# Kernel optimization log

Measured on AMD Instinct MI355X. Metric: run time of the kernel, lower is better.

## Reference

```python
import jax, jax.numpy as jnp
import numpy as np

T = 0.4       # gumbel temperature (self.T)
BASE = 3.0    # sigmoid offset (self.base)
LN_EPS = 1e-5


def setup_inputs() -> dict:
    key = jax.random.key(0)
    ks = jax.random.split(key, 4)
    B, S, D = 2, 2048, 4096
    E, EMB, M = 64, 128, 11008
    return {
        "x": jax.random.normal(ks[0], (B, S, D), dtype=jnp.float32),
        "rnn_state": jax.random.normal(ks[1], (E, EMB), dtype=jnp.float32),
        "Wr": jax.random.normal(ks[2], (E, D), dtype=jnp.float32) * 0.02,
        "Wd": jax.random.normal(ks[3], (M, EMB), dtype=jnp.float32) * 0.02,
        "ln_w": jnp.ones((EMB,), dtype=jnp.float32),
        "ln_b": jnp.zeros((EMB,), dtype=jnp.float32),
    }


def _layernorm(h, w, b):
    mu = jnp.mean(h, axis=-1, keepdims=True)
    var = jnp.var(h, axis=-1, keepdims=True)
    return (h - mu) * jax.lax.rsqrt(var + LN_EPS) * w + b


def reference(x, rnn_state, Wr, Wd, ln_w, ln_b):
    key = jax.random.key(42)
    k1, k2 = jax.random.split(key)
    # router logits: [B, S, E]
    logits = jnp.einsum("bsd,ed->bse", x, Wr)
    # ST gumbel-softmax (hard one-hot routing)
    eps = 1e-20
    u = jax.random.uniform(k1, logits.shape, dtype=logits.dtype)
    g = -jnp.log(-jnp.log(u + eps) + eps)
    y_soft = jax.nn.softmax((logits + g) / T, axis=-1)
    y_hard = jax.nn.one_hot(jnp.argmax(y_soft, axis=-1), logits.shape[-1], dtype=y_soft.dtype)
    router = jax.lax.stop_gradient(y_hard - y_soft) + y_soft
    # gather routed embedding: [B, S, EMB]
    routed = jnp.einsum("bse,ec->bsc", router, rnn_state)
    # LN + GELU (exact erf) + decode: [B, S, M]
    h = jax.nn.gelu(_layernorm(routed, ln_w, ln_b), approximate=False)
    pre = jnp.einsum("bsc,mc->bsm", h, Wd)
    # ST gumbel-sigmoid with offset, hard round
    e = jax.random.exponential(k2, pre.shape, dtype=pre.dtype)
    gum = -jnp.log(e)
    b_soft = jax.nn.sigmoid((pre + gum + BASE) / T)
    b_hard = jnp.round(b_soft)
    binary = jax.lax.stop_gradient(b_hard - b_soft) + b_soft
    return (binary, router)
```

## Files before the change

### kernel.cpp

```cpp
#include <hip/hip_runtime.h>
#include <hip/hip_bf16.h>
#include <stdint.h>

typedef float floatx4 __attribute__((ext_vector_type(4)));

__host__ __device__ inline void tf2x32(uint32_t k0, uint32_t k1,
                                       uint32_t x0, uint32_t x1,
                                       uint32_t& o0, uint32_t& o1) {
  const uint32_t k2 = k0 ^ k1 ^ 0x1BD11BDAu;
  x0 += k0; x1 += k1;
#define TFR(r) { x0 += x1; x1 = ((x1 << (r)) | (x1 >> (32 - (r)))); x1 ^= x0; }
  TFR(13) TFR(15) TFR(26) TFR(6)
  x0 += k1; x1 += k2 + 1u;
  TFR(17) TFR(29) TFR(16) TFR(24)
  x0 += k2; x1 += k0 + 2u;
  TFR(13) TFR(15) TFR(26) TFR(6)
  x0 += k0; x1 += k1 + 3u;
  TFR(17) TFR(29) TFR(16) TFR(24)
  x0 += k1; x1 += k2 + 4u;
  TFR(13) TFR(15) TFR(26) TFR(6)
  x0 += k2; x1 += k0 + 5u;
#undef TFR
  o0 = x0; o1 = x1;
}

__device__ inline uint32_t jax_bits32(uint32_t kA, uint32_t kB, uint32_t i) {
  uint32_t o0, o1;
  tf2x32(kA, kB, 0u, i, o0, o1);
  return o0 ^ o1;
}

__device__ inline float jax_uniform(uint32_t bits) {
  return __uint_as_float((bits >> 9) | 0x3f800000u) - 1.0f;
}

#define D_DIM   4096
#define E_DIM   64
#define EMB     128
#define M_DIM   11008
#define NROWS   4096
#define BIN_N   45088768
#define BK      32

__global__ __launch_bounds__(256) void krnA(const float* __restrict__ x,
                                            const float* __restrict__ Wr,
                                            float* __restrict__ part) {
  __shared__ float xs[64][BK + 1];
  __shared__ float wrs[64][BK + 1];
  const int rt = blockIdx.x, ks = blockIdx.y, t = threadIdx.x;
  const int row0 = rt * 64, k0 = ks * 1024;
  const int i = t >> 4, j = t & 15;
  float acc[4][4] = {};
  for (int kt = 0; kt < 1024; kt += BK) {
#pragma unroll
    for (int it = 0; it < 2; ++it) {
      int idx = t + it * 256;
      int r = idx >> 3, kq = idx & 7;
      float4 v = *(const float4*)&x[(size_t)(row0 + r) * D_DIM + k0 + kt + kq * 4];
      xs[r][kq * 4 + 0] = v.x; xs[r][kq * 4 + 1] = v.y;
      xs[r][kq * 4 + 2] = v.z; xs[r][kq * 4 + 3] = v.w;
      float4 w = *(const float4*)&Wr[(size_t)r * D_DIM + k0 + kt + kq * 4];
      wrs[r][kq * 4 + 0] = w.x; wrs[r][kq * 4 + 1] = w.y;
      wrs[r][kq * 4 + 2] = w.z; wrs[r][kq * 4 + 3] = w.w;
    }
    __syncthreads();
#pragma unroll
    for (int k = 0; k < BK; ++k) {
      float xv[4], wv[4];
#pragma unroll
      for (int c = 0; c < 4; ++c) xv[c] = xs[i * 4 + c][k];
#pragma unroll
      for (int d = 0; d < 4; ++d) wv[d] = wrs[j * 4 + d][k];
#pragma unroll
      for (int c = 0; c < 4; ++c)
#pragma unroll
        for (int d = 0; d < 4; ++d) acc[c][d] += xv[c] * wv[d];
    }
    __syncthreads();
  }
  float* pp = part + ((size_t)ks * NROWS + row0) * E_DIM;
#pragma unroll
  for (int c = 0; c < 4; ++c)
#pragma unroll
    for (int d = 0; d < 4; ++d)
      pp[(i * 4 + c) * E_DIM + j * 4 + d] = acc[c][d];
}

__global__ __launch_bounds__(256) void krnB(const float* __restrict__ part,
                                            float* __restrict__ router_out,
                                            int* __restrict__ eidx,
                                            uint32_t K1A, uint32_t K1B) {
  const int t = threadIdx.x;
  const int wv = t >> 6, lane = t & 63;
  const int row = blockIdx.x * 4 + wv;
  float lg = 0.0f;
#pragma unroll
  for (int s = 0; s < 4; ++s)
    lg += part[((size_t)s * NROWS + row) * E_DIM + lane];

  uint32_t jf = (uint32_t)row * 64u + (uint32_t)lane;
  uint32_t bits = jax_bits32(K1A, K1B, jf);
  float u = jax_uniform(bits);
  float inner = -logf(u + 1e-20f);
  float g = -logf(inner + 1e-20f);
  float w = (lg + g) * 2.5f;

  float m = w;
#pragma unroll
  for (int off = 32; off >= 1; off >>= 1) m = fmaxf(m, __shfl_xor(m, off));
  unsigned long long msk = __ballot(w == m);
  int arg = __ffsll(msk) - 1;
  router_out[(size_t)row * E_DIM + lane] = (lane == arg) ? 1.0f : 0.0f;
  if (lane == 0) eidx[row] = arg;
}

__global__ __launch_bounds__(64) void krnC1(const float* __restrict__ rnn,
                                            const float* __restrict__ lnw,
                                            const float* __restrict__ lnb,
                                            float* __restrict__ H) {
  const int r = blockIdx.x, lane = threadIdx.x;
  float v0 = rnn[r * EMB + lane], v1 = rnn[r * EMB + 64 + lane];
  float s = v0 + v1;
#pragma unroll
  for (int off = 32; off >= 1; off >>= 1) s += __shfl_xor(s, off);
  float mu = s * (1.0f / 128.0f);
  float d0 = v0 - mu, d1 = v1 - mu;
  float q = d0 * d0 + d1 * d1;
#pragma unroll
  for (int off = 32; off >= 1; off >>= 1) q += __shfl_xor(q, off);
  float var = q * (1.0f / 128.0f);
  float rs = rsqrtf(var + 1e-5f);
  float h0 = d0 * rs * lnw[lane] + lnb[lane];
  float h1 = d1 * rs * lnw[lane + 64] + lnb[lane + 64];
  float g0 = 0.5f * h0 * (1.0f + erff(h0 * 0.70710678118654752f));
  float g1 = 0.5f * h1 * (1.0f + erff(h1 * 0.70710678118654752f));
  H[r * EMB + lane] = g0;
  H[r * EMB + 64 + lane] = g1;
}

__global__ __launch_bounds__(256) void krnC2(const float* __restrict__ H,
                                             const float* __restrict__ Wd,
                                             float* __restrict__ P) {
  __shared__ float4 hs[64][32];
  const int t = threadIdx.x;
#pragma unroll
  for (int it = 0; it < 8; ++it) {
    int idx = t + it * 256;
    hs[idx >> 5][idx & 31] = ((const float4*)H)[idx];
  }
  __syncthreads();
  const int wv = t >> 6, lane = t & 63;
  const int m = blockIdx.x * 64 + lane;
  const float4* wd4 = (const float4*)(Wd + (size_t)m * EMB);
  float acc[16] = {};
  for (int c4 = 0; c4 < 32; ++c4) {
    float4 w = wd4[c4];
#pragma unroll
    for (int e = 0; e < 16; ++e) {
      float4 h = hs[wv * 16 + e][c4];
      acc[e] += w.x * h.x + w.y * h.y + w.z * h.z + w.w * h.w;
    }
  }
#pragma unroll
  for (int e = 0; e < 16; ++e)
    P[(size_t)(wv * 16 + e) * M_DIM + m] = acc[e];
}

__device__ inline float decide(float pre, uint32_t bits) {
  float u = jax_uniform(bits);
  float om = 1.0f - u;
  float e = -__logf(om);
  float gum = -__logf(e);
  float z = pre + gum + 3.0f;
  return (z > 0.0f) ? 1.0f : 0.0f;
}

__global__ __launch_bounds__(256) void krnD(const float* __restrict__ P,
                                            const int* __restrict__ eidx,
                                            float* __restrict__ out,
                                            uint32_t K2A, uint32_t K2B) {
  uint32_t g = (blockIdx.x * 256u + threadIdx.x) * 4u;
  uint32_t row = g / (uint32_t)M_DIM;
  uint32_t m = g - row * (uint32_t)M_DIM;
  int e = eidx[row];
  float4 pre = *(const float4*)&P[(size_t)e * M_DIM + m];
  floatx4 r;
  r.x = decide(pre.x, jax_bits32(K2A, K2B, g + 0u));
  r.y = decide(pre.y, jax_bits32(K2A, K2B, g + 1u));
  r.z = decide(pre.z, jax_bits32(K2A, K2B, g + 2u));
  r.w = decide(pre.w, jax_bits32(K2A, K2B, g + 3u));
  __builtin_nontemporal_store(r, (floatx4*)&out[g]);
}

extern "C" void kernel_launch(void* const* d_in, const int* in_sizes, int n_in,
                              void* d_out, int out_size, void* d_ws, size_t ws_size,
                              hipStream_t stream) {
  const float* x    = (const float*)d_in[0];
  const float* rnn  = (const float*)d_in[1];
  const float* Wr   = (const float*)d_in[2];
  const float* Wd   = (const float*)d_in[3];
  const float* lnw  = (const float*)d_in[4];
  const float* lnb  = (const float*)d_in[5];
  float* out = (float*)d_out;

  uint32_t K1A, K1B, K2A, K2B;
  tf2x32(0u, 42u, 0u, 0u, K1A, K1B);
  tf2x32(0u, 42u, 0u, 1u, K2A, K2B);

  char* ws = (char*)d_ws;
  float* part = (float*)ws;
  int*   eidx = (int*)(ws + 4194304);
  float* H    = (float*)(ws + 4194304 + 16384);
  float* P    = (float*)(ws + 4194304 + 16384 + 32768);

  float* router_out = out + (size_t)BIN_N;

  krnA<<<dim3(64, 4), 256, 0, stream>>>(x, Wr, part);
  krnB<<<1024, 256, 0, stream>>>(part, router_out, eidx, K1A, K1B);
  krnC1<<<64, 64, 0, stream>>>(rnn, lnw, lnb, H);
  krnC2<<<172, 256, 0, stream>>>(H, Wd, P);
  krnD<<<44032, 256, 0, stream>>>(P, eidx, out, K2A, K2B);
}
```

Measured before the change: 381.8 us.

## Retile router GEMM with wider split-K, skip decode loads via global min bound

```diff
diff --git a/kernel.cpp b/kernel.cpp
--- a/kernel.cpp
+++ b/kernel.cpp
@@ -3,13 +3,21 @@
 #include <stdint.h>
 
 typedef float floatx4 __attribute__((ext_vector_type(4)));
+
+__host__ __device__ inline uint32_t rotl32(uint32_t x, int r) {
+#ifdef __HIP_DEVICE_COMPILE__
+  return __builtin_amdgcn_alignbit(x, x, 32 - r);
+#else
+  return (x << r) | (x >> (32 - r));
+#endif
+}
 
 __host__ __device__ inline void tf2x32(uint32_t k0, uint32_t k1,
                                        uint32_t x0, uint32_t x1,
                                        uint32_t& o0, uint32_t& o1) {
   const uint32_t k2 = k0 ^ k1 ^ 0x1BD11BDAu;
   x0 += k0; x1 += k1;
-#define TFR(r) { x0 += x1; x1 = ((x1 << (r)) | (x1 >> (32 - (r)))); x1 ^= x0; }
+#define TFR(r) { x0 += x1; x1 = rotl32(x1, r); x1 ^= x0; }
   TFR(13) TFR(15) TFR(26) TFR(6)
   x0 += k1; x1 += k2 + 1u;
   TFR(17) TFR(29) TFR(16) TFR(24)
@@ -40,50 +48,70 @@
 #define M_DIM   11008
 #define NROWS   4096
 #define BIN_N   45088768
-#define BK      32
+#define KSPLIT  32
+#define CK      32
 
 __global__ __launch_bounds__(256) void krnA(const float* __restrict__ x,
                                             const float* __restrict__ Wr,
                                             float* __restrict__ part) {
-  __shared__ float xs[64][BK + 1];
-  __shared__ float wrs[64][BK + 1];
-  const int rt = blockIdx.x, ks = blockIdx.y, t = threadIdx.x;
-  const int row0 = rt * 64, k0 = ks * 1024;
-  const int i = t >> 4, j = t & 15;
-  float acc[4][4] = {};
-  for (int kt = 0; kt < 1024; kt += BK) {
+  __shared__ float xsT[CK * 256];
+  __shared__ float wsT[CK * 64];
+  const int rb = blockIdx.x, ks = blockIdx.y, t = threadIdx.x;
+  const int rbase = rb * 256, kbase0 = ks * 128;
+  const int jc = t & 7, rg = t >> 3;
+  float acc[8][8] = {};
+
+  for (int c = 0; c < 4; ++c) {
+    const int kbase = kbase0 + c * CK;
+#pragma unroll
+    for (int it = 0; it < 8; ++it) {
+      int idx = t + it * 256;
+      int row = idx >> 3, kq = idx & 7;
+      float4 v = *(const float4*)&x[(size_t)(rbase + row) * D_DIM + kbase + kq * 4];
+      int S = (kq & 3) << 3;
+      int r2 = row ^ S;
+      xsT[(kq * 4 + 0) * 256 + r2] = v.x;
+      xsT[(kq * 4 + 1) * 256 + r2] = v.y;
+      xsT[(kq * 4 + 2) * 256 + r2] = v.z;
+      xsT[(kq * 4 + 3) * 256 + r2] = v.w;
+    }
 #pragma unroll
     for (int it = 0; it < 2; ++it) {
       int idx = t + it * 256;
-      int r = idx >> 3, kq = idx & 7;
-      float4 v = *(const float4*)&x[(size_t)(row0 + r) * D_DIM + k0 + kt + kq * 4];
-      xs[r][kq * 4 + 0] = v.x; xs[r][kq * 4 + 1] = v.y;
-      xs[r][kq * 4 + 2] = v.z; xs[r][kq * 4 + 3] = v.w;
-      float4 w = *(const float4*)&Wr[(size_t)r * D_DIM + k0 + kt + kq * 4];
-      wrs[r][kq * 4 + 0] = w.x; wrs[r][kq * 4 + 1] = w.y;
-      wrs[r][kq * 4 + 2] = w.z; wrs[r][kq * 4 + 3] = w.w;
+      int e = idx >> 3, kq = idx & 7;
+      float4 v = *(const float4*)&Wr[(size_t)e * D_DIM + kbase + kq * 4];
+      int S = (kq & 3) << 3;
+      int e2 = e ^ S;
+      wsT[(kq * 4 + 0) * 64 + e2] = v.x;
+      wsT[(kq * 4 + 1) * 64 + e2] = v.y;
+      wsT[(kq * 4 + 2) * 64 + e2] = v.z;
+      wsT[(kq * 4 + 3) * 64 + e2] = v.w;
     }
     __syncthreads();
 #pragma unroll
-    for (int k = 0; k < BK; ++k) {
-      float xv[4], wv[4];
-#pragma unroll
-      for (int c = 0; c < 4; ++c) xv[c] = xs[i * 4 + c][k];
-#pragma unroll
-      for (int d = 0; d < 4; ++d) wv[d] = wrs[j * 4 + d][k];
-#pragma unroll
-      for (int c = 0; c < 4; ++c)
-#pragma unroll
-        for (int d = 0; d < 4; ++d) acc[c][d] += xv[c] * wv[d];
+    for (int k = 0; k < CK; ++k) {
+      int S = ((k >> 2) & 3) << 3;
+      const float* xp = &xsT[k * 256 + ((rg * 8) ^ S)];
+      const float* wp = &wsT[k * 64 + ((jc * 8) ^ S)];
+      floatx4 xa = *(const floatx4*)xp;
+      floatx4 xb = *(const floatx4*)(xp + 4);
+      floatx4 wa = *(const floatx4*)wp;
+      floatx4 wb = *(const floatx4*)(wp + 4);
+      float xv[8] = {xa.x, xa.y, xa.z, xa.w, xb.x, xb.y, xb.z, xb.w};
+      float wv[8] = {wa.x, wa.y, wa.z, wa.w, wb.x, wb.y, wb.z, wb.w};
+#pragma unroll
+      for (int r = 0; r < 8; ++r)
+#pragma unroll
+        for (int e = 0; e < 8; ++e) acc[r][e] += xv[r] * wv[e];
     }
     __syncthreads();
   }
-  float* pp = part + ((size_t)ks * NROWS + row0) * E_DIM;
-#pragma unroll
-  for (int c = 0; c < 4; ++c)
-#pragma unroll
-    for (int d = 0; d < 4; ++d)
-      pp[(i * 4 + c) * E_DIM + j * 4 + d] = acc[c][d];
+#pragma unroll
+  for (int r = 0; r < 8; ++r) {
+    float* pp = part + ((size_t)ks * NROWS + rbase + rg * 8 + r) * E_DIM + jc * 8;
+    *(float4*)pp = make_float4(acc[r][0], acc[r][1], acc[r][2], acc[r][3]);
+    *(float4*)(pp + 4) = make_float4(acc[r][4], acc[r][5], acc[r][6], acc[r][7]);
+  }
 }
 
 __global__ __launch_bounds__(256) void krnB(const float* __restrict__ part,
@@ -95,7 +123,7 @@
   const int row = blockIdx.x * 4 + wv;
   float lg = 0.0f;
 #pragma unroll
-  for (int s = 0; s < 4; ++s)
+  for (int s = 0; s < KSPLIT; ++s)
     lg += part[((size_t)s * NROWS + row) * E_DIM + lane];
 
   uint32_t jf = (uint32_t)row * 64u + (uint32_t)lane;
@@ -138,9 +166,15 @@
   H[r * EMB + 64 + lane] = g1;
 }
 
+__device__ inline uint32_t fkey(float f) {
+  uint32_t b = __float_as_uint(f);
+  return (b & 0x80000000u) ? ~b : (b | 0x80000000u);
+}
+
 __global__ __launch_bounds__(256) void krnC2(const float* __restrict__ H,
                                              const float* __restrict__ Wd,
-                                             float* __restrict__ P) {
+                                             float* __restrict__ P,
+                                             uint32_t* __restrict__ pminKey) {
   __shared__ float4 hs[64][32];
   const int t = threadIdx.x;
 #pragma unroll
@@ -161,9 +195,16 @@
       acc[e] += w.x * h.x + w.y * h.y + w.z * h.z + w.w * h.w;
     }
   }
-#pragma unroll
-  for (int e = 0; e < 16; ++e)
+  float mn = acc[0];
+#pragma unroll
+  for (int e = 0; e < 16; ++e) {
     P[(size_t)(wv * 16 + e) * M_DIM + m] = acc[e];
+    mn = fminf(mn, acc[e]);
+  }
+#pragma unroll
+  for (int off = 32; off >= 1; off >>= 1)
+    mn = fminf(mn, __shfl_xor(mn, off));
+  if (lane == 0) atomicMin(pminKey, fkey(mn));
 }
 
 __device__ inline float decide(float pre, uint32_t bits) {
@@ -177,18 +218,34 @@
 
 __global__ __launch_bounds__(256) void krnD(const float* __restrict__ P,
                                             const int* __restrict__ eidx,
+                                            const uint32_t* __restrict__ pminKey,
                                             float* __restrict__ out,
                                             uint32_t K2A, uint32_t K2B) {
+  uint32_t kk = *pminKey;
+  uint32_t pb = (kk & 0x80000000u) ? (kk ^ 0x80000000u) : ~kk;
+  float pmin = __uint_as_float(pb);
+  float tt = pmin + 2.95f;
+  float delta = __expf(-__expf(tt));
+  delta = fminf(fmaxf(delta, 1.2e-7f), 0.5f);
+  uint32_t Ku = (uint32_t)((1.0f - delta) * 8388608.0f);
+  uint32_t K9 = Ku << 9;
+
   uint32_t g = (blockIdx.x * 256u + threadIdx.x) * 4u;
-  uint32_t row = g / (uint32_t)M_DIM;
-  uint32_t m = g - row * (uint32_t)M_DIM;
-  int e = eidx[row];
-  float4 pre = *(const float4*)&P[(size_t)e * M_DIM + m];
-  floatx4 r;
-  r.x = decide(pre.x, jax_bits32(K2A, K2B, g + 0u));
-  r.y = decide(pre.y, jax_bits32(K2A, K2B, g + 1u));
-  r.z = decide(pre.z, jax_bits32(K2A, K2B, g + 2u));
-  r.w = decide(pre.w, jax_bits32(K2A, K2B, g + 3u));
+  uint32_t b0 = jax_bits32(K2A, K2B, g + 0u);
+  uint32_t b1 = jax_bits32(K2A, K2B, g + 1u);
+  uint32_t b2 = jax_bits32(K2A, K2B, g + 2u);
+  uint32_t b3 = jax_bits32(K2A, K2B, g + 3u);
+  floatx4 r = {1.0f, 1.0f, 1.0f, 1.0f};
+  uint32_t mx = max(max(b0, b1), max(b2, b3));
+  if (mx >= K9) {
+    uint32_t row = g / (uint32_t)M_DIM;
+    uint32_t m = g - row * (uint32_t)M_DIM;
+    const float* pp = &P[(size_t)eidx[row] * M_DIM + m];
+    if (b0 >= K9) r.x = decide(pp[0], b0);
+    if (b1 >= K9) r.y = decide(pp[1], b1);
+    if (b2 >= K9) r.z = decide(pp[2], b2);
+    if (b3 >= K9) r.w = decide(pp[3], b3);
+  }
   __builtin_nontemporal_store(r, (floatx4*)&out[g]);
 }
 
@@ -208,16 +265,18 @@
   tf2x32(0u, 42u, 0u, 1u, K2A, K2B);
 
   char* ws = (char*)d_ws;
-  float* part = (float*)ws;
-  int*   eidx = (int*)(ws + 4194304);
-  float* H    = (float*)(ws + 4194304 + 16384);
-  float* P    = (float*)(ws + 4194304 + 16384 + 32768);
-
+  int*      eidx    = (int*)ws;
+  float*    H       = (float*)(ws + 16384);
+  float*    P       = (float*)(ws + 65536);
+  uint32_t* pminKey = (uint32_t*)(ws + 3276800);
+
+  float* part = out;
   float* router_out = out + (size_t)BIN_N;
 
-  krnA<<<dim3(64, 4), 256, 0, stream>>>(x, Wr, part);
+  hipMemsetAsync(pminKey, 0xFF, 4, stream);
+  krnA<<<dim3(16, KSPLIT), 256, 0, stream>>>(x, Wr, part);
   krnB<<<1024, 256, 0, stream>>>(part, router_out, eidx, K1A, K1B);
   krnC1<<<64, 64, 0, stream>>>(rnn, lnw, lnb, H);
-  krnC2<<<172, 256, 0, stream>>>(H, Wd, P);
-  krnD<<<44032, 256, 0, stream>>>(P, eidx, out, K2A, K2B);
-}
+  krnC2<<<172, 256, 0, stream>>>(H, Wd, P, pminKey);
+  krnD<<<44032, 256, 0, stream>>>(P, eidx, pminKey, out, K2A, K2B);
+}
```

New measurement: 335.0 us. -12.3%, faster.
